# Performance work log

Measured on AMD Instinct MI355X. Metric: run time of the kernel, lower is better.

Reference implementation:

```python
import jax, jax.numpy as jnp
import numpy as np

BLOCK = (16, 16)  # (block rows over out_features, block cols over in_features)
TOKENS, IN_F, OUT_F = 8192, 4096, 4096


def setup_inputs() -> dict:
    key = jax.random.key(0)
    k1, k2, k3, k4 = jax.random.split(key, 4)
    x = jax.random.normal(k1, (TOKENS, IN_F), dtype=jnp.float32)
    weight = jax.random.normal(k2, (OUT_F, IN_F), dtype=jnp.float32) / np.sqrt(IN_F)
    bias = jax.random.normal(k3, (OUT_F,), dtype=jnp.float32)
    block_mask = jax.random.bernoulli(k4, 0.5, (OUT_F // BLOCK[0], IN_F // BLOCK[1]))
    return {"x": x, "weight": weight, "bias": bias, "block_mask": block_mask}


def _expand_mask(block_mask, dtype):
    # [X, Y] block mask -> [out_features, in_features] dense 0/1 mask
    m = jnp.repeat(block_mask, BLOCK[0], axis=0)
    m = jnp.repeat(m, BLOCK[1], axis=1)
    return m.astype(dtype)


def reference(x, weight, bias, block_mask):
    # Sparse path: block-sparse matmul with the block-masked weight
    # (blocksparseMM(sparse_data, x, block_size) == x @ (W * mask).T)
    w_sparse = weight * _expand_mask(block_mask, weight.dtype)
    x_sparse = jnp.einsum('ti,oi->to', x, w_sparse)
    # Dense residual path: standard linear with the full weight + bias
    x_dense = jnp.einsum('ti,oi->to', x, weight) + bias
    return x_sparse + x_dense
```

## Files before the change

### kernel.cpp

```cpp
#include <hip/hip_runtime.h>
#include <hip/hip_bf16.h>
#include <stdint.h>

#define TOKENS 8192
#define IN_F   4096
#define OUT_F  4096

typedef __attribute__((ext_vector_type(4))) float  f32x4;
typedef __attribute__((ext_vector_type(8))) __bf16 bf16x8;

__device__ __forceinline__ unsigned short f2bf(float f) {
    union { float f; uint32_t u; } c; c.f = f;
    uint32_t u = c.u;
    u += 0x7fffu + ((u >> 16) & 1);
    return (unsigned short)(u >> 16);
}

__device__ __forceinline__ void load_lds_16(const void* gptr, void* lptr) {
    __builtin_amdgcn_global_load_lds(
        (const __attribute__((address_space(1))) unsigned int*)gptr,
        (__attribute__((address_space(3))) unsigned int*)lptr, 16, 0, 0);
}

template<int N> __device__ __forceinline__ void vm_bar() {
    if constexpr (N == 4) asm volatile("s_waitcnt vmcnt(4)\ns_barrier" ::: "memory");
    else                  asm volatile("s_waitcnt vmcnt(0)\ns_barrier" ::: "memory");
}
template<int N> __device__ __forceinline__ void lgkm() {
    if constexpr (N == 8)      asm volatile("s_waitcnt lgkmcnt(8)" ::: "memory");
    else if constexpr (N == 4) asm volatile("s_waitcnt lgkmcnt(4)" ::: "memory");
    else                       asm volatile("s_waitcnt lgkmcnt(0)" ::: "memory");
    __builtin_amdgcn_sched_barrier(0);
}

#define XBLOCKS 2048
#define WBLOCKS 1024
__global__ __launch_bounds__(256) void cvt_kernel(const float* __restrict__ x,
                                                  const float* __restrict__ w,
                                                  const int* __restrict__ mask,
                                                  unsigned short* __restrict__ xb,
                                                  unsigned short* __restrict__ wb) {
    int b = blockIdx.x;
    if (b < XBLOCKS) {
        const int n4 = TOKENS * IN_F / 4;
        int i = b * 256 + threadIdx.x;
        const int stride = XBLOCKS * 256;
        for (; i < n4; i += stride) {
            float4 v = ((const float4*)x)[i];
            ushort4 o;
            o.x = f2bf(v.x); o.y = f2bf(v.y); o.z = f2bf(v.z); o.w = f2bf(v.w);
            ((ushort4*)xb)[i] = o;
        }
    } else {
        const int n4 = OUT_F * IN_F / 4;
        int i = (b - XBLOCKS) * 256 + threadIdx.x;
        const int stride = WBLOCKS * 256;
        for (; i < n4; i += stride) {
            int elem = i * 4;
            int o = elem >> 12;
            int k = elem & (IN_F - 1);
            int mb = mask[(o >> 4) * (IN_F / 16) + (k >> 4)];
            float s = mb ? 2.0f : 1.0f;
            float4 v = ((const float4*)w)[i];
            ushort4 ov;
            ov.x = f2bf(v.x * s); ov.y = f2bf(v.y * s);
            ov.z = f2bf(v.z * s); ov.w = f2bf(v.w * s);
            ((ushort4*)wb)[i] = ov;
        }
    }
}

#define BM 256
#define BN 256
#define BK 64
#define NT (IN_F / BK)

#define ST_A(T, H) {                                                           \
    const unsigned short* s_ = srcA + (size_t)(T) * BK + (H) * 32;             \
    unsigned short* d_ = sm + (((T) & 1) * 16384 + (H) * 8192) + dstL;         \
    load_lds_16(s_, d_);                                                       \
    load_lds_16(s_ + (size_t)128 * IN_F, d_ + 4096); }
#define ST_B(T, H) {                                                           \
    const unsigned short* s_ = srcB + (size_t)(T) * BK + (H) * 32;             \
    unsigned short* d_ = sm + (32768 + ((T) & 1) * 16384 + (H) * 8192) + dstL; \
    load_lds_16(s_, d_);                                                       \
    load_lds_16(s_ + (size_t)128 * IN_F, d_ + 4096); }

#define RDB4(R0, R1, R2, R3, BUF, KS) {                                        \
    const unsigned short* p_ = sm + 32768 + (BUF) * 16384 + (KS) * 8192 + b_base; \
    R0 = *(const bf16x8*)(p_);        R1 = *(const bf16x8*)(p_ + 512);         \
    R2 = *(const bf16x8*)(p_ + 1024); R3 = *(const bf16x8*)(p_ + 1536); }

#define RDA4(R0, R1, R2, R3, BUF, KS, MH) {                                    \
    const unsigned short* p_ = sm + (BUF) * 16384 + (KS) * 8192 + (MH) * 2048 + a_base; \
    R0 = *(const bf16x8*)(p_);        R1 = *(const bf16x8*)(p_ + 512);         \
    R2 = *(const bf16x8*)(p_ + 1024); R3 = *(const bf16x8*)(p_ + 1536); }

#define MM16(A0, A1, A2, A3, B0, B1, B2, B3, MH) {                             \
    __builtin_amdgcn_s_setprio(1);                                             \
    acc[(MH)*4+0][0] = __builtin_amdgcn_mfma_f32_16x16x32_bf16(A0, B0, acc[(MH)*4+0][0], 0, 0, 0); \
    acc[(MH)*4+0][1] = __builtin_amdgcn_mfma_f32_16x16x32_bf16(A0, B1, acc[(MH)*4+0][1], 0, 0, 0); \
    acc[(MH)*4+0][2] = __builtin_amdgcn_mfma_f32_16x16x32_bf16(A0, B2, acc[(MH)*4+0][2], 0, 0, 0); \
    acc[(MH)*4+0][3] = __builtin_amdgcn_mfma_f32_16x16x32_bf16(A0, B3, acc[(MH)*4+0][3], 0, 0, 0); \
    acc[(MH)*4+1][0] = __builtin_amdgcn_mfma_f32_16x16x32_bf16(A1, B0, acc[(MH)*4+1][0], 0, 0, 0); \
    acc[(MH)*4+1][1] = __builtin_amdgcn_mfma_f32_16x16x32_bf16(A1, B1, acc[(MH)*4+1][1], 0, 0, 0); \
    acc[(MH)*4+1][2] = __builtin_amdgcn_mfma_f32_16x16x32_bf16(A1, B2, acc[(MH)*4+1][2], 0, 0, 0); \
    acc[(MH)*4+1][3] = __builtin_amdgcn_mfma_f32_16x16x32_bf16(A1, B3, acc[(MH)*4+1][3], 0, 0, 0); \
    acc[(MH)*4+2][0] = __builtin_amdgcn_mfma_f32_16x16x32_bf16(A2, B0, acc[(MH)*4+2][0], 0, 0, 0); \
    acc[(MH)*4+2][1] = __builtin_amdgcn_mfma_f32_16x16x32_bf16(A2, B1, acc[(MH)*4+2][1], 0, 0, 0); \
    acc[(MH)*4+2][2] = __builtin_amdgcn_mfma_f32_16x16x32_bf16(A2, B2, acc[(MH)*4+2][2], 0, 0, 0); \
    acc[(MH)*4+2][3] = __builtin_amdgcn_mfma_f32_16x16x32_bf16(A2, B3, acc[(MH)*4+2][3], 0, 0, 0); \
    acc[(MH)*4+3][0] = __builtin_amdgcn_mfma_f32_16x16x32_bf16(A3, B0, acc[(MH)*4+3][0], 0, 0, 0); \
    acc[(MH)*4+3][1] = __builtin_amdgcn_mfma_f32_16x16x32_bf16(A3, B1, acc[(MH)*4+3][1], 0, 0, 0); \
    acc[(MH)*4+3][2] = __builtin_amdgcn_mfma_f32_16x16x32_bf16(A3, B2, acc[(MH)*4+3][2], 0, 0, 0); \
    acc[(MH)*4+3][3] = __builtin_amdgcn_mfma_f32_16x16x32_bf16(A3, B3, acc[(MH)*4+3][3], 0, 0, 0); \
    __builtin_amdgcn_s_setprio(0); }

__global__ __launch_bounds__(512, 2) void gemm8_kernel(const unsigned short* __restrict__ A,
                                                       const unsigned short* __restrict__ B,
                                                       const float* __restrict__ bias,
                                                       float* __restrict__ C) {
    extern __shared__ __align__(16) unsigned short sm[];

    const int tid  = threadIdx.x;
    const int lane = tid & 63;
    const int wid  = tid >> 6;
    const int wr   = wid >> 2;
    const int wc   = wid & 3;

    const int nwg = (TOKENS / BM) * (OUT_F / BN);
    int bid = blockIdx.x;
    int swz = (bid & 7) * (nwg >> 3) + (bid >> 3);
    const int tiles_n = OUT_F / BN;
    const int t0 = (swz / tiles_n) * BM;
    const int o0 = (swz % tiles_n) * BN;

    const int srow = tid >> 2;
    const int sc   = tid & 3;
    const int scs  = sc ^ ((srow >> 1) & 3);
    const unsigned short* srcA = A + (size_t)(t0 + srow) * IN_F + scs * 8;
    const unsigned short* srcB = B + (size_t)(o0 + srow) * IN_F + scs * 8;
    const int dstL = srow * 32 + sc * 8;

    const int l15 = lane & 15, q = lane >> 4;
    const int qe = q ^ ((l15 >> 1) & 3);
    const int a_base = (wr * 128 + l15) * 32 + qe * 8;
    const int b_base = (wc * 64 + l15) * 32 + qe * 8;

    f32x4 acc[8][4];
#pragma unroll
    for (int i = 0; i < 8; ++i)
#pragma unroll
        for (int j = 0; j < 4; ++j) acc[i][j] = (f32x4)0.0f;

    bf16x8 aaE0, aaE1, aaE2, aaE3, aaO0, aaO1, aaO2, aaO3;
    bf16x8 bbE0, bbE1, bbE2, bbE3, bbO0, bbO1, bbO2, bbO3;

    ST_A(0, 0) ST_B(0, 0) ST_A(0, 1) ST_B(0, 1)
    vm_bar<4>();
    RDB4(bbE0, bbE1, bbE2, bbE3, 0, 0)
    RDA4(aaE0, aaE1, aaE2, aaE3, 0, 0, 0)

#pragma unroll 1
    for (int T = 0; T < NT - 1; ++T) {
        const int bc = T & 1, nbc = bc ^ 1;
        ST_A(T + 1, 0)
        RDA4(aaO0, aaO1, aaO2, aaO3, bc, 0, 1)
        lgkm<4>();
        MM16(aaE0, aaE1, aaE2, aaE3, bbE0, bbE1, bbE2, bbE3, 0)
        ST_B(T + 1, 0)
        vm_bar<4>();
        RDB4(bbO0, bbO1, bbO2, bbO3, bc, 1)
        RDA4(aaE0, aaE1, aaE2, aaE3, bc, 1, 0)
        lgkm<8>();
        MM16(aaO0, aaO1, aaO2, aaO3, bbE0, bbE1, bbE2, bbE3, 1)
        ST_A(T + 1, 1)
        RDA4(aaO0, aaO1, aaO2, aaO3, bc, 1, 1)
        lgkm<4>();
        MM16(aaE0, aaE1, aaE2, aaE3, bbO0, bbO1, bbO2, bbO3, 0)
        ST_B(T + 1, 1)
        vm_bar<4>();
        RDB4(bbE0, bbE1, bbE2, bbE3, nbc, 0)
        RDA4(aaE0, aaE1, aaE2, aaE3, nbc, 0, 0)
        lgkm<8>();
        MM16(aaO0, aaO1, aaO2, aaO3, bbO0, bbO1, bbO2, bbO3, 1)
    }
    {
        RDA4(aaO0, aaO1, aaO2, aaO3, 1, 0, 1)
        lgkm<4>();
        MM16(aaE0, aaE1, aaE2, aaE3, bbE0, bbE1, bbE2, bbE3, 0)
        vm_bar<0>();
        RDB4(bbO0, bbO1, bbO2, bbO3, 1, 1)
        RDA4(aaE0, aaE1, aaE2, aaE3, 1, 1, 0)
        lgkm<8>();
        MM16(aaO0, aaO1, aaO2, aaO3, bbE0, bbE1, bbE2, bbE3, 1)
        RDA4(aaO0, aaO1, aaO2, aaO3, 1, 1, 1)
        lgkm<4>();
        MM16(aaE0, aaE1, aaE2, aaE3, bbO0, bbO1, bbO2, bbO3, 0)
        lgkm<0>();
        MM16(aaO0, aaO1, aaO2, aaO3, bbO0, bbO1, bbO2, bbO3, 1)
    }

    float bv[4];
#pragma unroll
    for (int nf = 0; nf < 4; ++nf) bv[nf] = bias[o0 + wc * 64 + nf * 16 + l15];
#pragma unroll
    for (int mf = 0; mf < 8; ++mf) {
        const int t = t0 + wr * 128 + mf * 16 + q * 4;
#pragma unroll
        for (int nf = 0; nf < 4; ++nf) {
            const int o = o0 + wc * 64 + nf * 16 + l15;
#pragma unroll
            for (int r = 0; r < 4; ++r)
                C[(size_t)(t + r) * OUT_F + o] = acc[mf][nf][r] + bv[nf];
        }
    }
}

__global__ __launch_bounds__(256) void gemm_f32_fallback(const float* __restrict__ x,
                                                         const float* __restrict__ w,
                                                         const float* __restrict__ bias,
                                                         const int* __restrict__ mask,
                                                         float* __restrict__ out) {
    __shared__ float As[64][17];
    __shared__ float Bs[64][17];
    int bid = blockIdx.x;
    const int tiles_n = OUT_F / 64;
    int tm = bid / tiles_n, tn = bid % tiles_n;
    int t0 = tm * 64, o0 = tn * 64;
    int tid = threadIdx.x;
    int tx = tid & 15, ty = tid >> 4;
    int lrow = tid >> 2, lc4 = (tid & 3) * 4;
    float acc[4][4] = {};
    for (int k0 = 0; k0 < IN_F; k0 += 16) {
        float4 av = *(const float4*)&x[(size_t)(t0 + lrow) * IN_F + k0 + lc4];
        float4 bv = *(const float4*)&w[(size_t)(o0 + lrow) * IN_F + k0 + lc4];
        int mb = mask[((o0 + lrow) >> 4) * (IN_F / 16) + ((k0 + lc4) >> 4)];
        float s = mb ? 2.0f : 1.0f;
        As[lrow][lc4 + 0] = av.x; As[lrow][lc4 + 1] = av.y;
        As[lrow][lc4 + 2] = av.z; As[lrow][lc4 + 3] = av.w;
        Bs[lrow][lc4 + 0] = bv.x * s; Bs[lrow][lc4 + 1] = bv.y * s;
        Bs[lrow][lc4 + 2] = bv.z * s; Bs[lrow][lc4 + 3] = bv.w * s;
        __syncthreads();
#pragma unroll
        for (int kk = 0; kk < 16; ++kk) {
            float av2[4], bv2[4];
#pragma unroll
            for (int i = 0; i < 4; ++i) av2[i] = As[ty * 4 + i][kk];
#pragma unroll
            for (int j = 0; j < 4; ++j) bv2[j] = Bs[tx * 4 + j][kk];
#pragma unroll
            for (int i = 0; i < 4; ++i)
#pragma unroll
                for (int j = 0; j < 4; ++j) acc[i][j] += av2[i] * bv2[j];
        }
        __syncthreads();
    }
#pragma unroll
    for (int j = 0; j < 4; ++j) {
        int o = o0 + tx * 4 + j;
        float bv = bias[o];
#pragma unroll
        for (int i = 0; i < 4; ++i)
            out[(size_t)(t0 + ty * 4 + i) * OUT_F + o] = acc[i][j] + bv;
    }
}

extern "C" void kernel_launch(void* const* d_in, const int* in_sizes, int n_in,
                              void* d_out, int out_size, void* d_ws, size_t ws_size,
                              hipStream_t stream) {
    const float* x    = (const float*)d_in[0];
    const float* wgt  = (const float*)d_in[1];
    const float* bias = (const float*)d_in[2];
    const int*   mask = (const int*)d_in[3];
    float* out = (float*)d_out;

    size_t xb_bytes = (size_t)TOKENS * IN_F * 2;
    size_t wb_bytes = (size_t)OUT_F * IN_F * 2;

    if (ws_size >= xb_bytes + wb_bytes) {
        unsigned short* xb = (unsigned short*)d_ws;
        unsigned short* wb = (unsigned short*)((char*)d_ws + xb_bytes);
        hipLaunchKernelGGL(cvt_kernel, dim3(XBLOCKS + WBLOCKS), dim3(256), 0, stream,
                           x, wgt, mask, xb, wb);
        (void)hipFuncSetAttribute((const void*)gemm8_kernel,
                                  hipFuncAttributeMaxDynamicSharedMemorySize, 131072);
        hipLaunchKernelGGL(gemm8_kernel, dim3((TOKENS / BM) * (OUT_F / BN)), dim3(512),
                           131072, stream, xb, wb, bias, out);
    } else {
        hipLaunchKernelGGL(gemm_f32_fallback, dim3((TOKENS / 64) * (OUT_F / 64)), dim3(256), 0, stream,
                           x, wgt, bias, mask, out);
    }
}
```

Measured before the change: 288.8 us.

## Restructure GEMM main loop to issue whole-tile prefetch after single barrier

Replaces the finely interleaved half-tile prefetch schedule, which used partial vmcnt waits and two barriers per K-tile, with one full barrier per tile. After that barrier the next tile's A and B global-to-LDS loads are all issued up front, then the current tile is read from LDS and fed to the MFMAs. The aim is fewer barriers and simpler scheduling. The cost is that the next tile's loads are no longer staggered against compute, so each barrier waits for vmcnt(0), which can expose global-load latency.

```diff
diff --git a/kernel.cpp b/kernel.cpp
--- a/kernel.cpp
+++ b/kernel.cpp
@@ -22,9 +22,9 @@
         (__attribute__((address_space(3))) unsigned int*)lptr, 16, 0, 0);
 }
 
-template<int N> __device__ __forceinline__ void vm_bar() {
-    if constexpr (N == 4) asm volatile("s_waitcnt vmcnt(4)\ns_barrier" ::: "memory");
-    else                  asm volatile("s_waitcnt vmcnt(0)\ns_barrier" ::: "memory");
+__device__ __forceinline__ void tile_bar() {
+    asm volatile("s_waitcnt vmcnt(0)\ns_barrier" ::: "memory");
+    __builtin_amdgcn_sched_barrier(0);
 }
 template<int N> __device__ __forceinline__ void lgkm() {
     if constexpr (N == 8)      asm volatile("s_waitcnt lgkmcnt(8)" ::: "memory");
@@ -116,6 +116,24 @@
     acc[(MH)*4+3][3] = __builtin_amdgcn_mfma_f32_16x16x32_bf16(A3, B3, acc[(MH)*4+3][3], 0, 0, 0); \
     __builtin_amdgcn_s_setprio(0); }
 
+#define BODY(BC)                                                               \
+  {                                                                            \
+    RDB4(bbE0, bbE1, bbE2, bbE3, BC, 0)                                        \
+    RDA4(aaE0, aaE1, aaE2, aaE3, BC, 0, 0)                                     \
+    RDA4(aaO0, aaO1, aaO2, aaO3, BC, 0, 1)                                     \
+    lgkm<4>();                                                                 \
+    MM16(aaE0, aaE1, aaE2, aaE3, bbE0, bbE1, bbE2, bbE3, 0)                    \
+    RDB4(bbO0, bbO1, bbO2, bbO3, BC, 1)                                        \
+    RDA4(aaE0, aaE1, aaE2, aaE3, BC, 1, 0)                                     \
+    lgkm<8>();                                                                 \
+    MM16(aaO0, aaO1, aaO2, aaO3, bbE0, bbE1, bbE2, bbE3, 1)                    \
+    RDA4(aaO0, aaO1, aaO2, aaO3, BC, 1, 1)                                     \
+    lgkm<4>();                                                                 \
+    MM16(aaE0, aaE1, aaE2, aaE3, bbO0, bbO1, bbO2, bbO3, 0)                    \
+    lgkm<0>();                                                                 \
+    MM16(aaO0, aaO1, aaO2, aaO3, bbO0, bbO1, bbO2, bbO3, 1)                    \
+  }
+
 __global__ __launch_bounds__(512, 2) void gemm8_kernel(const unsigned short* __restrict__ A,
                                                        const unsigned short* __restrict__ B,
                                                        const float* __restrict__ bias,
@@ -157,48 +175,17 @@
     bf16x8 bbE0, bbE1, bbE2, bbE3, bbO0, bbO1, bbO2, bbO3;
 
     ST_A(0, 0) ST_B(0, 0) ST_A(0, 1) ST_B(0, 1)
-    vm_bar<4>();
-    RDB4(bbE0, bbE1, bbE2, bbE3, 0, 0)
-    RDA4(aaE0, aaE1, aaE2, aaE3, 0, 0, 0)
 
 #pragma unroll 1
     for (int T = 0; T < NT - 1; ++T) {
-        const int bc = T & 1, nbc = bc ^ 1;
-        ST_A(T + 1, 0)
-        RDA4(aaO0, aaO1, aaO2, aaO3, bc, 0, 1)
-        lgkm<4>();
-        MM16(aaE0, aaE1, aaE2, aaE3, bbE0, bbE1, bbE2, bbE3, 0)
-        ST_B(T + 1, 0)
-        vm_bar<4>();
-        RDB4(bbO0, bbO1, bbO2, bbO3, bc, 1)
-        RDA4(aaE0, aaE1, aaE2, aaE3, bc, 1, 0)
-        lgkm<8>();
-        MM16(aaO0, aaO1, aaO2, aaO3, bbE0, bbE1, bbE2, bbE3, 1)
-        ST_A(T + 1, 1)
-        RDA4(aaO0, aaO1, aaO2, aaO3, bc, 1, 1)
-        lgkm<4>();
-        MM16(aaE0, aaE1, aaE2, aaE3, bbO0, bbO1, bbO2, bbO3, 0)
-        ST_B(T + 1, 1)
-        vm_bar<4>();
-        RDB4(bbE0, bbE1, bbE2, bbE3, nbc, 0)
-        RDA4(aaE0, aaE1, aaE2, aaE3, nbc, 0, 0)
-        lgkm<8>();
-        MM16(aaO0, aaO1, aaO2, aaO3, bbO0, bbO1, bbO2, bbO3, 1)
-    }
-    {
-        RDA4(aaO0, aaO1, aaO2, aaO3, 1, 0, 1)
-        lgkm<4>();
-        MM16(aaE0, aaE1, aaE2, aaE3, bbE0, bbE1, bbE2, bbE3, 0)
-        vm_bar<0>();
-        RDB4(bbO0, bbO1, bbO2, bbO3, 1, 1)
-        RDA4(aaE0, aaE1, aaE2, aaE3, 1, 1, 0)
-        lgkm<8>();
-        MM16(aaO0, aaO1, aaO2, aaO3, bbE0, bbE1, bbE2, bbE3, 1)
-        RDA4(aaO0, aaO1, aaO2, aaO3, 1, 1, 1)
-        lgkm<4>();
-        MM16(aaE0, aaE1, aaE2, aaE3, bbO0, bbO1, bbO2, bbO3, 0)
-        lgkm<0>();
-        MM16(aaO0, aaO1, aaO2, aaO3, bbO0, bbO1, bbO2, bbO3, 1)
+        const int bc = T & 1;
+        tile_bar();
+        ST_A(T + 1, 0) ST_B(T + 1, 0) ST_A(T + 1, 1) ST_B(T + 1, 1)
+        BODY(bc)
+    }
+    {   const int bc = (NT - 1) & 1;
+        tile_bar();
+        BODY(bc)
     }
 
     float bv[4];
```

Result: slower. 299.9 us (+3.8%).
